# Optimization experiments

Hardware: AMD Instinct MI355X
Metric: run time of the kernel (lower is better)

Reference implementation:

```python
import jax, jax.numpy as jnp
import numpy as np

DIM = 1024
NUM_HEADS = 16


def setup_inputs() -> dict:
    key = jax.random.key(0)
    ks = jax.random.split(key, 6)
    B, N, C = 2, 2048, DIM
    x = jax.random.normal(ks[0], (B, N, C), dtype=jnp.float32)
    # torch nn.Linear weights have shape (out, in); qkv_bias=False, proj has bias
    wq = jax.random.normal(ks[1], (C, C), dtype=jnp.float32) * 0.02
    wk = jax.random.normal(ks[2], (C, C), dtype=jnp.float32) * 0.02
    wv = jax.random.normal(ks[3], (C, C), dtype=jnp.float32) * 0.02
    wp = jax.random.normal(ks[4], (C, C), dtype=jnp.float32) * 0.02
    bp = jax.random.normal(ks[5], (C,), dtype=jnp.float32) * 0.02
    return {"x": x, "wq": wq, "wk": wk, "wv": wv, "wp": wp, "bp": bp}


def reference(x, wq, wk, wv, wp, bp):
    B, N, C = x.shape
    H = NUM_HEADS
    D = C // H
    scale = D ** (-0.5)
    # projections (torch Linear: x @ W.T), split heads -> (B, H, N, D)
    q = (x @ wq.T).reshape(B, N, H, D).transpose(0, 2, 1, 3)
    k = (x @ wk.T).reshape(B, N, H, D).transpose(0, 2, 1, 3)
    v = (x @ wv.T).reshape(B, N, H, D).transpose(0, 2, 1, 3)
    # average keys over sequence -> (B, H, D)
    k_avg = k.mean(axis=2)
    # per-position logits against the single averaged key -> (B, H, N)
    z = jnp.einsum('bhnd,bhd->bhn', q, k_avg) * scale
    attn = jax.nn.softmax(z, axis=-1)  # (B, H, N); dropout is identity at eval
    # build circulant matrix: roll_weights[..., i, j] = attn[..., (j - i) mod N]
    pos = jnp.arange(N)
    idx = (pos[None, :] - pos[:, None]) % N  # (N, N)
    roll_weights = attn[:, :, idx]  # (B, H, N, N) gather-built circulant
    out = jnp.einsum('bhij,bhjd->bhid', roll_weights, v)  # (B, H, N, D)
    out = out.transpose(0, 2, 1, 3).reshape(B, N, C)
    return out @ wp.T + bp
```

## Files before the change

### kernel.cpp

```cpp
#include <hip/hip_runtime.h>
#include <stdint.h>

typedef unsigned short u16;
typedef __bf16 bf16x8 __attribute__((ext_vector_type(8)));
typedef float f32x4 __attribute__((ext_vector_type(4)));

static constexpr int kDim   = 1024;
static constexpr int kHeads = 16;
static constexpr int kN     = 2048;
static constexpr int kB     = 2;
static constexpr int kTok   = 4096;

static constexpr size_t OFF_XB   = 0;
static constexpr size_t OFF_VT   = OFF_XB   + (size_t)kTok*kDim*2;
static constexpr size_t OFF_OC   = OFF_VT   + (size_t)kTok*kDim*2;
static constexpr size_t OFF_WVB  = OFF_OC   + (size_t)kTok*kDim*2;
static constexpr size_t OFF_WPB  = OFF_WVB  + (size_t)kDim*kDim*2;
static constexpr size_t OFF_XSUM = OFF_WPB  + (size_t)kDim*kDim*2;
static constexpr size_t OFF_WZ   = OFF_XSUM + (size_t)kB*kDim*4;
static constexpr size_t OFF_Z    = OFF_WZ   + (size_t)kB*kHeads*kDim*4;
static constexpr size_t OFF_ATTN = OFF_Z    + (size_t)kB*kHeads*kN*4;
static constexpr int kAttnStride = 2064;

__device__ __forceinline__ u16 f2bf(float f) {
  unsigned int u = __builtin_bit_cast(unsigned int, f);
  u = (u + 0x7FFFu + ((u >> 16) & 1u)) >> 16;
  return (u16)u;
}

__device__ __forceinline__ void gload_lds16(const void* g, void* l) {
  __builtin_amdgcn_global_load_lds(
      (const __attribute__((address_space(1))) unsigned int*)g,
      (__attribute__((address_space(3))) unsigned int*)l, 16, 0, 0);
}

__global__ void cvt_bf16_kernel(const float* __restrict__ in, u16* __restrict__ out, int n4) {
  int i = blockIdx.x * 256 + threadIdx.x;
  if (i < n4) {
    float4 f = reinterpret_cast<const float4*>(in)[i];
    u16 a = f2bf(f.x), b = f2bf(f.y), c = f2bf(f.z), d = f2bf(f.w);
    unsigned int lo = (unsigned int)a | ((unsigned int)b << 16);
    unsigned int hi = (unsigned int)c | ((unsigned int)d << 16);
    reinterpret_cast<uint2*>(out)[i] = make_uint2(lo, hi);
  }
}

__global__ void xsum_kernel(const float* __restrict__ x, float* __restrict__ xsum) {
  int bid = blockIdx.x;
  int cc = bid & 3, nc = (bid >> 2) & 15, b = bid >> 6;
  int c = cc * 256 + threadIdx.x;
  const float* xp = x + ((size_t)b * kN + nc * 128) * kDim + c;
  float s = 0.f;
  for (int n = 0; n < 128; ++n) s += xp[(size_t)n * kDim];
  atomicAdd(&xsum[b * kDim + c], s);
}

__global__ void kavgwz_kernel(const float* __restrict__ xsum, const float* __restrict__ wk,
                              const float* __restrict__ wq, float* __restrict__ wz) {
  int bh = blockIdx.x;
  int b = bh >> 4, h = bh & 15, tid = threadIdx.x;
  __shared__ float kl[64];
  int d = tid >> 2, part = tid & 3;
  const float* wkr = wk + (size_t)(h * 64 + d) * kDim;
  const float* xs = xsum + b * kDim;
  float s = 0.f;
  for (int k = part; k < kDim; k += 4) s += xs[k] * wkr[k];
  s += __shfl_xor(s, 1);
  s += __shfl_xor(s, 2);
  if (part == 0) kl[d] = s * (1.0f / (float)kN);
  __syncthreads();
  float a0 = 0.f, a1 = 0.f, a2 = 0.f, a3 = 0.f;
  const float* wqb = wq + (size_t)h * 64 * kDim + tid;
  for (int dd = 0; dd < 64; ++dd) {
    float kd = kl[dd];
    const float* r = wqb + (size_t)dd * kDim;
    a0 += kd * r[0]; a1 += kd * r[256]; a2 += kd * r[512]; a3 += kd * r[768];
  }
  const float scale = 0.125f;
  float* o = wz + (size_t)bh * kDim + tid;
  o[0] = a0 * scale; o[256] = a1 * scale; o[512] = a2 * scale; o[768] = a3 * scale;
}

__global__ void z_kernel(const float* __restrict__ x, const float* __restrict__ wz,
                         float* __restrict__ z) {
  int blk = blockIdx.x;
  int b = blk >> 11, n = blk & 2047;
  __shared__ float xr[kDim];
  int tid = threadIdx.x, wid = tid >> 6, lane = tid & 63;
  reinterpret_cast<float4*>(xr)[tid] = reinterpret_cast<const float4*>(x + (size_t)blk * kDim)[tid];
  __syncthreads();
#pragma unroll
  for (int hh = 0; hh < 4; ++hh) {
    int h = wid * 4 + hh;
    const float* wzr = wz + (size_t)(b * kHeads + h) * kDim;
    float s = 0.f;
    for (int k = lane; k < kDim; k += 64) s += xr[k] * wzr[k];
#pragma unroll
    for (int off = 32; off; off >>= 1) s += __shfl_xor(s, off);
    if (lane == 0) z[(size_t)(b * kHeads + h) * kN + n] = s;
  }
}

__global__ void softmax_kernel(const float* __restrict__ z, u16* __restrict__ attn2) {
  int row = blockIdx.x, tid = threadIdx.x;
  int lane = tid & 63, wid = tid >> 6;
  const float* zr = z + (size_t)row * kN;
  float v[8];
  float mx = -1e30f;
#pragma unroll
  for (int j = 0; j < 8; ++j) { v[j] = zr[tid + j * 256]; mx = fmaxf(mx, v[j]); }
#pragma unroll
  for (int off = 32; off; off >>= 1) mx = fmaxf(mx, __shfl_xor(mx, off));
  __shared__ float redm[4], reds[4];
  if (lane == 0) redm[wid] = mx;
  __syncthreads();
  mx = fmaxf(fmaxf(redm[0], redm[1]), fmaxf(redm[2], redm[3]));
  float s = 0.f;
#pragma unroll
  for (int j = 0; j < 8; ++j) { v[j] = __expf(v[j] - mx); s += v[j]; }
#pragma unroll
  for (int off = 32; off; off >>= 1) s += __shfl_xor(s, off);
  if (lane == 0) reds[wid] = s;
  __syncthreads();
  s = reds[0] + reds[1] + reds[2] + reds[3];
  float inv = 1.0f / s;
  u16* out = attn2 + (size_t)row * kAttnStride;
#pragma unroll
  for (int j = 0; j < 8; ++j) out[tid + j * 256] = f2bf(v[j] * inv);
  if (tid < 8) out[2048 + tid] = f2bf(v[0] * inv);
}

template <int MODE>
__global__ __launch_bounds__(256, 2)
void gemm_bt_kernel(const u16* __restrict__ A, const u16* __restrict__ B,
                    void* __restrict__ Cout, const float* __restrict__ bias, int K) {
  __shared__ __align__(16) u16 As[2][128 * 64];
  __shared__ __align__(16) u16 Bs[2][128 * 64];
  int tid = threadIdx.x, lane = tid & 63, wid = tid >> 6;
  int wm = wid >> 1, wn = wid & 1;
  int lrow = lane & 15, kg = lane >> 4;
  int m0 = blockIdx.y * 128, n0 = blockIdx.x * 128;

  auto stage = [&](int buf, int k0) {
#pragma unroll
    for (int it = 0; it < 4; ++it) {
      int bchunk = it * 256 + wid * 64;
      int chunk = bchunk + lane;
      int row = chunk >> 3, cb = chunk & 7;
      int cs = cb ^ (row & 7);
      gload_lds16(A + (size_t)(m0 + row) * K + k0 + cs * 8, &As[buf][bchunk * 8]);
    }
#pragma unroll
    for (int it = 0; it < 4; ++it) {
      int bchunk = it * 256 + wid * 64;
      int chunk = bchunk + lane;
      int row = chunk >> 3, cb = chunk & 7;
      int cs = cb ^ (row & 7);
      gload_lds16(B + (size_t)(n0 + row) * K + k0 + cs * 8, &Bs[buf][bchunk * 8]);
    }
  };

  f32x4 acc[4][4];
#pragma unroll
  for (int i = 0; i < 4; ++i)
#pragma unroll
    for (int j = 0; j < 4; ++j) acc[i][j] = (f32x4){0.f, 0.f, 0.f, 0.f};

  stage(0, 0);
  __syncthreads();
  int buf = 0;
  for (int k0 = 0; k0 < K; k0 += 64) {
    if (k0 + 64 < K) stage(buf ^ 1, k0 + 64);
#pragma unroll
    for (int ks = 0; ks < 2; ++ks) {
      bf16x8 af[4], bfv[4];
#pragma unroll
      for (int mf = 0; mf < 4; ++mf) {
        int r = wm * 64 + mf * 16 + lrow;
        int c = (ks * 4 + kg) ^ (r & 7);
        af[mf] = *reinterpret_cast<const bf16x8*>(&As[buf][r * 64 + c * 8]);
      }
#pragma unroll
      for (int nf = 0; nf < 4; ++nf) {
        int r = wn * 64 + nf * 16 + lrow;
        int c = (ks * 4 + kg) ^ (r & 7);
        bfv[nf] = *reinterpret_cast<const bf16x8*>(&Bs[buf][r * 64 + c * 8]);
      }
#pragma unroll
      for (int mf = 0; mf < 4; ++mf)
#pragma unroll
        for (int nf = 0; nf < 4; ++nf)
          acc[mf][nf] = __builtin_amdgcn_mfma_f32_16x16x32_bf16(af[mf], bfv[nf], acc[mf][nf], 0, 0, 0);
    }
    __syncthreads();
    buf ^= 1;
  }

  if (MODE == 0) {
    u16* vT = (u16*)Cout;
#pragma unroll
    for (int mf = 0; mf < 4; ++mf) {
      int row0 = m0 + wm * 64 + mf * 16 + kg * 4;
      int bb = row0 >> 11, u = row0 & 2047;
#pragma unroll
      for (int nf = 0; nf < 4; ++nf) {
        int col = n0 + wn * 64 + nf * 16 + lrow;
        f32x4 a = acc[mf][nf];
        unsigned int lo = (unsigned int)f2bf(a.x) | ((unsigned int)f2bf(a.y) << 16);
        unsigned int hi = (unsigned int)f2bf(a.z) | ((unsigned int)f2bf(a.w) << 16);
        *reinterpret_cast<uint2*>(&vT[((size_t)(bb * kDim + col)) * kN + u]) = make_uint2(lo, hi);
      }
    }
  } else {
    float* y = (float*)Cout;
#pragma unroll
    for (int nf = 0; nf < 4; ++nf) {
      int col = n0 + wn * 64 + nf * 16 + lrow;
      float bv = bias[col];
#pragma unroll
      for (int mf = 0; mf < 4; ++mf) {
        int row0 = m0 + wm * 64 + mf * 16 + kg * 4;
        f32x4 a = acc[mf][nf];
        y[(size_t)(row0 + 0) * kDim + col] = a.x + bv;
        y[(size_t)(row0 + 1) * kDim + col] = a.y + bv;
        y[(size_t)(row0 + 2) * kDim + col] = a.z + bv;
        y[(size_t)(row0 + 3) * kDim + col] = a.w + bv;
      }
    }
  }
}

__global__ __launch_bounds__(256, 2)
void conv_kernel(const u16* __restrict__ vT, const u16* __restrict__ attn2,
                 u16* __restrict__ oc) {
  static constexpr int RS = 2056;
  __shared__ __align__(16) u16 reps[8 * RS];
  __shared__ __align__(16) u16 vts[2][64 * 64];
  int tid = threadIdx.x, lane = tid & 63, wid = tid >> 6;
  int wm = wid >> 1, wn = wid & 1;
  int lrow = lane & 15, kg = lane >> 4;
  int bh = blockIdx.x;
  int i0 = blockIdx.y * 128;
  int b = bh >> 4, h = bh & 15;

  const u16* arow = attn2 + (size_t)bh * kAttnStride;
  for (int p = 0; p < 8; ++p)
    for (int j = tid; j < 2048; j += 256) reps[p * RS + j] = arow[j + p];

  auto stage = [&](int buf, int u0) {
#pragma unroll
    for (int it = 0; it < 2; ++it) {
      int bchunk = it * 256 + wid * 64;
      int chunk = bchunk + lane;
      int d = chunk >> 3, cb = chunk & 7;
      int cs = cb ^ (d & 7);
      gload_lds16(vT + (size_t)(bh * 64 + d) * kN + u0 + cs * 8, &vts[buf][bchunk * 8]);
    }
  };

  f32x4 acc[2][4];
#pragma unroll
  for (int i = 0; i < 2; ++i)
#pragma unroll
    for (int j = 0; j < 4; ++j) acc[i][j] = (f32x4){0.f, 0.f, 0.f, 0.f};

  stage(0, 0);
  __syncthreads();
  int buf = 0;
  for (int u0 = 0; u0 < kN; u0 += 64) {
    if (u0 + 64 < kN) stage(buf ^ 1, u0 + 64);
#pragma unroll
    for (int ks = 0; ks < 2; ++ks) {
      bf16x8 af[2], bfv[4];
#pragma unroll
      for (int mf = 0; mf < 2; ++mf) {
        int r = wm * 32 + mf * 16 + lrow;
        int c = (ks * 4 + kg) ^ (r & 7);
        af[mf] = *reinterpret_cast<const bf16x8*>(&vts[buf][r * 64 + c * 8]);
      }
#pragma unroll
      for (int nf = 0; nf < 4; ++nf) {
        int i = i0 + wn * 64 + nf * 16 + lrow;
        int s = (u0 + ks * 32 + kg * 8 - i) & 2047;
        int p = s & 7;
        bfv[nf] = *reinterpret_cast<const bf16x8*>(&reps[p * RS + (s & ~7)]);
      }
#pragma unroll
      for (int mf = 0; mf < 2; ++mf)
#pragma unroll
        for (int nf = 0; nf < 4; ++nf)
          acc[mf][nf] = __builtin_amdgcn_mfma_f32_16x16x32_bf16(af[mf], bfv[nf], acc[mf][nf], 0, 0, 0);
    }
    __syncthreads();
    buf ^= 1;
  }

#pragma unroll
  for (int mf = 0; mf < 2; ++mf) {
    int d = wm * 32 + mf * 16 + kg * 4;
#pragma unroll
    for (int nf = 0; nf < 4; ++nf) {
      int i = i0 + wn * 64 + nf * 16 + lrow;
      f32x4 a = acc[mf][nf];
      unsigned int lo = (unsigned int)f2bf(a.x) | ((unsigned int)f2bf(a.y) << 16);
      unsigned int hi = (unsigned int)f2bf(a.z) | ((unsigned int)f2bf(a.w) << 16);
      *reinterpret_cast<uint2*>(&oc[((size_t)(b * kN + i)) * kDim + h * 64 + d]) = make_uint2(lo, hi);
    }
  }
}

extern "C" void kernel_launch(void* const* d_in, const int* in_sizes, int n_in,
                              void* d_out, int out_size, void* d_ws, size_t ws_size,
                              hipStream_t stream) {
  const float* x  = (const float*)d_in[0];
  const float* wq = (const float*)d_in[1];
  const float* wk = (const float*)d_in[2];
  const float* wv = (const float*)d_in[3];
  const float* wp = (const float*)d_in[4];
  const float* bp = (const float*)d_in[5];
  char* ws = (char*)d_ws;

  u16*   xb    = (u16*)(ws + OFF_XB);
  u16*   vTb   = (u16*)(ws + OFF_VT);
  u16*   ocb   = (u16*)(ws + OFF_OC);
  u16*   wvb   = (u16*)(ws + OFF_WVB);
  u16*   wpb   = (u16*)(ws + OFF_WPB);
  float* xsum  = (float*)(ws + OFF_XSUM);
  float* wz    = (float*)(ws + OFF_WZ);
  float* z     = (float*)(ws + OFF_Z);
  u16*   attn2 = (u16*)(ws + OFF_ATTN);

  hipMemsetAsync(ws + OFF_XSUM, 0, (size_t)kB * kDim * 4, stream);

  cvt_bf16_kernel<<<4096, 256, 0, stream>>>(x,  xb,  kTok * kDim / 4);
  cvt_bf16_kernel<<<1024, 256, 0, stream>>>(wv, wvb, kDim * kDim / 4);
  cvt_bf16_kernel<<<1024, 256, 0, stream>>>(wp, wpb, kDim * kDim / 4);

  xsum_kernel<<<128, 256, 0, stream>>>(x, xsum);
  kavgwz_kernel<<<32, 256, 0, stream>>>(xsum, wk, wq, wz);
  z_kernel<<<4096, 256, 0, stream>>>(x, wz, z);
  softmax_kernel<<<32, 256, 0, stream>>>(z, attn2);

  gemm_bt_kernel<0><<<dim3(8, 32), 256, 0, stream>>>(xb, wvb, vTb, nullptr, kDim);
  conv_kernel<<<dim3(32, 16), 256, 0, stream>>>(vTb, attn2, ocb);
  gemm_bt_kernel<1><<<dim3(8, 32), 256, 0, stream>>>(ocb, wpb, (float*)d_out, bp, kDim);
}
```

Baseline: 239.5 us.

## Fuse x conversion with column sums, merge weight casts, shrink GEMM N-tile

Fuses the x-to-bf16 conversion with the per-chunk column sums, writing partial sums instead of using atomics plus a memset. It merges the two weight conversions into one launch, relying on wpb sitting right after wvb in the workspace. The GEMM N-tile drops from 128 to 64, doubling the grid to 512 blocks for better CU coverage at the cost of less A-tile reuse. The conv grid axes are swapped so blocks sharing a head are launched next to each other.

```diff
diff --git a/kernel.cpp b/kernel.cpp
--- a/kernel.cpp
+++ b/kernel.cpp
@@ -16,8 +16,8 @@
 static constexpr size_t OFF_OC   = OFF_VT   + (size_t)kTok*kDim*2;
 static constexpr size_t OFF_WVB  = OFF_OC   + (size_t)kTok*kDim*2;
 static constexpr size_t OFF_WPB  = OFF_WVB  + (size_t)kDim*kDim*2;
-static constexpr size_t OFF_XSUM = OFF_WPB  + (size_t)kDim*kDim*2;
-static constexpr size_t OFF_WZ   = OFF_XSUM + (size_t)kB*kDim*4;
+static constexpr size_t OFF_PART = OFF_WPB  + (size_t)kDim*kDim*2;
+static constexpr size_t OFF_WZ   = OFF_PART + (size_t)kB*16*kDim*4;
 static constexpr size_t OFF_Z    = OFF_WZ   + (size_t)kB*kHeads*kDim*4;
 static constexpr size_t OFF_ATTN = OFF_Z    + (size_t)kB*kHeads*kN*4;
 static constexpr int kAttnStride = 2064;
@@ -34,40 +34,61 @@
       (__attribute__((address_space(3))) unsigned int*)l, 16, 0, 0);
 }
 
-__global__ void cvt_bf16_kernel(const float* __restrict__ in, u16* __restrict__ out, int n4) {
-  int i = blockIdx.x * 256 + threadIdx.x;
-  if (i < n4) {
-    float4 f = reinterpret_cast<const float4*>(in)[i];
-    u16 a = f2bf(f.x), b = f2bf(f.y), c = f2bf(f.z), d = f2bf(f.w);
-    unsigned int lo = (unsigned int)a | ((unsigned int)b << 16);
-    unsigned int hi = (unsigned int)c | ((unsigned int)d << 16);
-    reinterpret_cast<uint2*>(out)[i] = make_uint2(lo, hi);
-  }
-}
-
-__global__ void xsum_kernel(const float* __restrict__ x, float* __restrict__ xsum) {
+__global__ void cvtx_xsum_kernel(const float* __restrict__ x, u16* __restrict__ xb,
+                                 float* __restrict__ part) {
   int bid = blockIdx.x;
   int cc = bid & 3, nc = (bid >> 2) & 15, b = bid >> 6;
-  int c = cc * 256 + threadIdx.x;
-  const float* xp = x + ((size_t)b * kN + nc * 128) * kDim + c;
-  float s = 0.f;
-  for (int n = 0; n < 128; ++n) s += xp[(size_t)n * kDim];
-  atomicAdd(&xsum[b * kDim + c], s);
-}
-
-__global__ void kavgwz_kernel(const float* __restrict__ xsum, const float* __restrict__ wk,
+  int tid = threadIdx.x, rg = tid >> 6, cl = tid & 63;
+  int col = cc * 256 + cl * 4;
+  size_t base = (size_t)b * kN + nc * 128;
+  float4 s = make_float4(0.f, 0.f, 0.f, 0.f);
+  for (int n = rg; n < 128; n += 4) {
+    size_t idx = (base + n) * kDim + col;
+    float4 v = *reinterpret_cast<const float4*>(&x[idx]);
+    unsigned int lo = (unsigned int)f2bf(v.x) | ((unsigned int)f2bf(v.y) << 16);
+    unsigned int hi = (unsigned int)f2bf(v.z) | ((unsigned int)f2bf(v.w) << 16);
+    *reinterpret_cast<uint2*>(&xb[idx]) = make_uint2(lo, hi);
+    s.x += v.x; s.y += v.y; s.z += v.z; s.w += v.w;
+  }
+  __shared__ float ps[4][256];
+  ps[rg][cl * 4 + 0] = s.x; ps[rg][cl * 4 + 1] = s.y;
+  ps[rg][cl * 4 + 2] = s.z; ps[rg][cl * 4 + 3] = s.w;
+  __syncthreads();
+  float tot = ps[0][tid] + ps[1][tid] + ps[2][tid] + ps[3][tid];
+  part[((size_t)(b * 16 + nc)) * kDim + cc * 256 + tid] = tot;
+}
+
+__global__ void cvtw_kernel(const float* __restrict__ wv, const float* __restrict__ wp,
+                            u16* __restrict__ out) {
+  int i = blockIdx.x * 256 + threadIdx.x;
+  const int half = kDim * kDim / 4;
+  float4 f = (i < half) ? reinterpret_cast<const float4*>(wv)[i]
+                        : reinterpret_cast<const float4*>(wp)[i - half];
+  unsigned int lo = (unsigned int)f2bf(f.x) | ((unsigned int)f2bf(f.y) << 16);
+  unsigned int hi = (unsigned int)f2bf(f.z) | ((unsigned int)f2bf(f.w) << 16);
+  reinterpret_cast<uint2*>(out)[i] = make_uint2(lo, hi);
+}
+
+__global__ void kavgwz_kernel(const float* __restrict__ part, const float* __restrict__ wk,
                               const float* __restrict__ wq, float* __restrict__ wz) {
   int bh = blockIdx.x;
   int b = bh >> 4, h = bh & 15, tid = threadIdx.x;
+  __shared__ float xsl[1024];
   __shared__ float kl[64];
-  int d = tid >> 2, part = tid & 3;
+  {
+    f32x4 s = (f32x4){0.f, 0.f, 0.f, 0.f};
+    for (int ch = 0; ch < 16; ++ch)
+      s += *reinterpret_cast<const f32x4*>(&part[((size_t)(b * 16 + ch)) * kDim + tid * 4]);
+    *reinterpret_cast<f32x4*>(&xsl[tid * 4]) = s;
+  }
+  __syncthreads();
+  int d = tid >> 2, pt = tid & 3;
   const float* wkr = wk + (size_t)(h * 64 + d) * kDim;
-  const float* xs = xsum + b * kDim;
   float s = 0.f;
-  for (int k = part; k < kDim; k += 4) s += xs[k] * wkr[k];
+  for (int k = pt; k < kDim; k += 4) s += xsl[k] * wkr[k];
   s += __shfl_xor(s, 1);
   s += __shfl_xor(s, 2);
-  if (part == 0) kl[d] = s * (1.0f / (float)kN);
+  if (pt == 0) kl[d] = s * (1.0f / (float)kN);
   __syncthreads();
   float a0 = 0.f, a1 = 0.f, a2 = 0.f, a3 = 0.f;
   const float* wqb = wq + (size_t)h * 64 * kDim + tid;
@@ -135,11 +156,11 @@
 void gemm_bt_kernel(const u16* __restrict__ A, const u16* __restrict__ B,
                     void* __restrict__ Cout, const float* __restrict__ bias, int K) {
   __shared__ __align__(16) u16 As[2][128 * 64];
-  __shared__ __align__(16) u16 Bs[2][128 * 64];
+  __shared__ __align__(16) u16 Bs[2][64 * 64];
   int tid = threadIdx.x, lane = tid & 63, wid = tid >> 6;
   int wm = wid >> 1, wn = wid & 1;
   int lrow = lane & 15, kg = lane >> 4;
-  int m0 = blockIdx.y * 128, n0 = blockIdx.x * 128;
+  int m0 = blockIdx.y * 128, n0 = blockIdx.x * 64;
 
   auto stage = [&](int buf, int k0) {
 #pragma unroll
@@ -151,7 +172,7 @@
       gload_lds16(A + (size_t)(m0 + row) * K + k0 + cs * 8, &As[buf][bchunk * 8]);
     }
 #pragma unroll
-    for (int it = 0; it < 4; ++it) {
+    for (int it = 0; it < 2; ++it) {
       int bchunk = it * 256 + wid * 64;
       int chunk = bchunk + lane;
       int row = chunk >> 3, cb = chunk & 7;
@@ -160,11 +181,11 @@
     }
   };
 
-  f32x4 acc[4][4];
+  f32x4 acc[4][2];
 #pragma unroll
   for (int i = 0; i < 4; ++i)
 #pragma unroll
-    for (int j = 0; j < 4; ++j) acc[i][j] = (f32x4){0.f, 0.f, 0.f, 0.f};
+    for (int j = 0; j < 2; ++j) acc[i][j] = (f32x4){0.f, 0.f, 0.f, 0.f};
 
   stage(0, 0);
   __syncthreads();
@@ -173,7 +194,7 @@
     if (k0 + 64 < K) stage(buf ^ 1, k0 + 64);
 #pragma unroll
     for (int ks = 0; ks < 2; ++ks) {
-      bf16x8 af[4], bfv[4];
+      bf16x8 af[4], bfv[2];
 #pragma unroll
       for (int mf = 0; mf < 4; ++mf) {
         int r = wm * 64 + mf * 16 + lrow;
@@ -181,15 +202,15 @@
         af[mf] = *reinterpret_cast<const bf16x8*>(&As[buf][r * 64 + c * 8]);
       }
 #pragma unroll
-      for (int nf = 0; nf < 4; ++nf) {
-        int r = wn * 64 + nf * 16 + lrow;
+      for (int nf = 0; nf < 2; ++nf) {
+        int r = wn * 32 + nf * 16 + lrow;
         int c = (ks * 4 + kg) ^ (r & 7);
         bfv[nf] = *reinterpret_cast<const bf16x8*>(&Bs[buf][r * 64 + c * 8]);
       }
 #pragma unroll
       for (int mf = 0; mf < 4; ++mf)
 #pragma unroll
-        for (int nf = 0; nf < 4; ++nf)
+        for (int nf = 0; nf < 2; ++nf)
           acc[mf][nf] = __builtin_amdgcn_mfma_f32_16x16x32_bf16(af[mf], bfv[nf], acc[mf][nf], 0, 0, 0);
     }
     __syncthreads();
@@ -203,8 +224,8 @@
       int row0 = m0 + wm * 64 + mf * 16 + kg * 4;
       int bb = row0 >> 11, u = row0 & 2047;
 #pragma unroll
-      for (int nf = 0; nf < 4; ++nf) {
-        int col = n0 + wn * 64 + nf * 16 + lrow;
+      for (int nf = 0; nf < 2; ++nf) {
+        int col = n0 + wn * 32 + nf * 16 + lrow;
         f32x4 a = acc[mf][nf];
         unsigned int lo = (unsigned int)f2bf(a.x) | ((unsigned int)f2bf(a.y) << 16);
         unsigned int hi = (unsigned int)f2bf(a.z) | ((unsigned int)f2bf(a.w) << 16);
@@ -214,8 +235,8 @@
   } else {
     float* y = (float*)Cout;
 #pragma unroll
-    for (int nf = 0; nf < 4; ++nf) {
-      int col = n0 + wn * 64 + nf * 16 + lrow;
+    for (int nf = 0; nf < 2; ++nf) {
+      int col = n0 + wn * 32 + nf * 16 + lrow;
       float bv = bias[col];
 #pragma unroll
       for (int mf = 0; mf < 4; ++mf) {
@@ -239,8 +260,8 @@
   int tid = threadIdx.x, lane = tid & 63, wid = tid >> 6;
   int wm = wid >> 1, wn = wid & 1;
   int lrow = lane & 15, kg = lane >> 4;
-  int bh = blockIdx.x;
-  int i0 = blockIdx.y * 128;
+  int i0 = blockIdx.x * 128;
+  int bh = blockIdx.y;
   int b = bh >> 4, h = bh & 15;
 
   const u16* arow = attn2 + (size_t)bh * kAttnStride;
@@ -324,24 +345,19 @@
   u16*   vTb   = (u16*)(ws + OFF_VT);
   u16*   ocb   = (u16*)(ws + OFF_OC);
   u16*   wvb   = (u16*)(ws + OFF_WVB);
-  u16*   wpb   = (u16*)(ws + OFF_WPB);
-  float* xsum  = (float*)(ws + OFF_XSUM);
+  float* part  = (float*)(ws + OFF_PART);
   float* wz    = (float*)(ws + OFF_WZ);
   float* z     = (float*)(ws + OFF_Z);
   u16*   attn2 = (u16*)(ws + OFF_ATTN);
-
-  hipMemsetAsync(ws + OFF_XSUM, 0, (size_t)kB * kDim * 4, stream);
-
-  cvt_bf16_kernel<<<4096, 256, 0, stream>>>(x,  xb,  kTok * kDim / 4);
-  cvt_bf16_kernel<<<1024, 256, 0, stream>>>(wv, wvb, kDim * kDim / 4);
-  cvt_bf16_kernel<<<1024, 256, 0, stream>>>(wp, wpb, kDim * kDim / 4);
-
-  xsum_kernel<<<128, 256, 0, stream>>>(x, xsum);
-  kavgwz_kernel<<<32, 256, 0, stream>>>(xsum, wk, wq, wz);
+  u16*   wpb   = (u16*)(ws + OFF_WPB);
+
+  cvtx_xsum_kernel<<<128, 256, 0, stream>>>(x, xb, part);
+  cvtw_kernel<<<2048, 256, 0, stream>>>(wv, wp, wvb);
+  kavgwz_kernel<<<32, 256, 0, stream>>>(part, wk, wq, wz);
   z_kernel<<<4096, 256, 0, stream>>>(x, wz, z);
   softmax_kernel<<<32, 256, 0, stream>>>(z, attn2);
 
-  gemm_bt_kernel<0><<<dim3(8, 32), 256, 0, stream>>>(xb, wvb, vTb, nullptr, kDim);
-  conv_kernel<<<dim3(32, 16), 256, 0, stream>>>(vTb, attn2, ocb);
-  gemm_bt_kernel<1><<<dim3(8, 32), 256, 0, stream>>>(ocb, wpb, (float*)d_out, bp, kDim);
-}
+  gemm_bt_kernel<0><<<dim3(16, 32), 256, 0, stream>>>(xb, wvb, vTb, nullptr, kDim);
+  conv_kernel<<<dim3(16, 32), 256, 0, stream>>>(vTb, attn2, ocb);
+  gemm_bt_kernel<1><<<dim3(16, 32), 256, 0, stream>>>(ocb, wpb, (float*)d_out, bp, kDim);
+}
```

Result: faster. 230.1 us (-3.9%).
